# Kernel optimization log

Hardware: AMD Instinct MI355X
Metric: run time of the kernel (lower is better)

## Reference

```python
import jax, jax.numpy as jnp
import numpy as np

T, B, IN, H = 256, 256, 512, 512


def setup_inputs() -> dict:
    key = jax.random.key(0)
    k_x, k_d, k_ih, k_hh = jax.random.split(key, 4)
    x = jax.random.normal(k_x, (T, B, IN), dtype=jnp.float32)
    dones = jax.random.randint(k_d, (T, B), 0, 2, dtype=jnp.int32)
    # xavier_normal_ init as in the torch module (biases filled with 0)
    s_ih = (2.0 / (4 * H + IN)) ** 0.5
    s_hh = (2.0 / (4 * H + H)) ** 0.5
    W_ih = jax.random.normal(k_ih, (4 * H, IN), dtype=jnp.float32) * s_ih
    W_hh = jax.random.normal(k_hh, (4 * H, H), dtype=jnp.float32) * s_hh
    b_ih = jnp.zeros((4 * H,), dtype=jnp.float32)
    b_hh = jnp.zeros((4 * H,), dtype=jnp.float32)
    return {"x": x, "dones": dones, "W_ih": W_ih, "W_hh": W_hh,
            "b_ih": b_ih, "b_hh": b_hh}


def _lstm_scan(x, dones, W_ih, W_hh, b_ih, b_hh):
    # x: [T, B, IN], dones: [T, B]; single-layer LSTM, zero initial state.
    Bn = x.shape[1]
    Hn = W_hh.shape[1]
    h0 = jnp.zeros((Bn, Hn), dtype=x.dtype)
    c0 = jnp.zeros((Bn, Hn), dtype=x.dtype)
    b = b_ih + b_hh

    def step(carry, inp):
        h, c = carry
        x_t, d_t = inp
        keep = (1.0 - d_t.astype(x_t.dtype))[:, None]  # reset state where done
        h = h * keep
        c = c * keep
        pre = jnp.stack([h, c])  # [2, B, H] = concat(hidden, cell) before step
        gates = x_t @ W_ih.T + h @ W_hh.T + b  # [B, 4H], torch order i,f,g,o
        i, f, g, o = jnp.split(gates, 4, axis=-1)
        c_new = jax.nn.sigmoid(f) * c + jax.nn.sigmoid(i) * jnp.tanh(g)
        h_new = jax.nn.sigmoid(o) * jnp.tanh(c_new)
        return (h_new, c_new), (h_new, pre)

    _, (lstm_outputs, hidden_outputs) = jax.lax.scan(step, (h0, c0), (x, dones))
    # lstm_outputs: [T, B, H]; hidden_outputs: [T, 2*num_layers, B, H]
    return lstm_outputs, hidden_outputs


def reference(x, dones, W_ih, W_hh, b_ih, b_hh):
    return _lstm_scan(x, dones, W_ih, W_hh, b_ih, b_hh)
```

## Files before the change

### kernel.cpp

```cpp
#include <hip/hip_runtime.h>


#define T_STEPS 256
#define BATCH   256
#define INP     512
#define HID     512
#define GROUPS  8
#define MEMB    32
#define BT      32
#define NWG     (GROUPS*MEMB)
#define NTHR    256
#define XBUF    65536
#define K8OFF   (2*XBUF)
#define LDS_BYTES (2*XBUF + T_STEPS*BT)
#define PARM    0x40004000u

typedef float  f32x4  __attribute__((ext_vector_type(4)));
typedef short  bf16x8 __attribute__((ext_vector_type(8)));
typedef unsigned int u32x4 __attribute__((ext_vector_type(4)));

struct HF { u32x4 h[16]; };

typedef const __attribute__((address_space(1))) void gas_v;
typedef __attribute__((address_space(3))) void las_v;
__device__ __forceinline__ void gld_lds16(const void* g, void* l) {
  __builtin_amdgcn_global_load_lds((gas_v*)g, (las_v*)l, 16, 0, 0);
}

__device__ __forceinline__ unsigned short f2bf(float f) {
  unsigned u = __builtin_bit_cast(unsigned, f);
  return (unsigned short)((u + 0x8000u) >> 16);
}
__device__ __forceinline__ bf16x8 cvt8(float4 a, float4 b) {
  bf16x8 v;
  v[0]=(short)f2bf(a.x); v[1]=(short)f2bf(a.y); v[2]=(short)f2bf(a.z); v[3]=(short)f2bf(a.w);
  v[4]=(short)f2bf(b.x); v[5]=(short)f2bf(b.y); v[6]=(short)f2bf(b.z); v[7]=(short)f2bf(b.w);
  return v;
}
__device__ __forceinline__ float sigf(float x) {
  return __fdividef(1.0f, 1.0f + __expf(-x));
}
__device__ __forceinline__ float tanh_(float x) {
  float e = __expf(-2.0f * fabsf(x));
  float t = __fdividef(1.0f - e, 1.0f + e);
  return copysignf(t, x);
}
__device__ __forceinline__ f32x4 shflx4(f32x4 v, int m) {
  f32x4 r;
  r[0]=__shfl_xor(v[0],m,64); r[1]=__shfl_xor(v[1],m,64);
  r[2]=__shfl_xor(v[2],m,64); r[3]=__shfl_xor(v[3],m,64);
  return r;
}

__device__ __forceinline__ void llc_load_h(HF& o, const void* p) {
  unsigned long long a = (unsigned long long)p;
  asm volatile(
    "global_load_dwordx4 %[h0],  %[a], off sc0 sc1\n\t"
    "global_load_dwordx4 %[h1],  %[a], off offset:64 sc0 sc1\n\t"
    "global_load_dwordx4 %[h2],  %[a], off offset:128 sc0 sc1\n\t"
    "global_load_dwordx4 %[h3],  %[a], off offset:192 sc0 sc1\n\t"
    "global_load_dwordx4 %[h4],  %[a], off offset:256 sc0 sc1\n\t"
    "global_load_dwordx4 %[h5],  %[a], off offset:320 sc0 sc1\n\t"
    "global_load_dwordx4 %[h6],  %[a], off offset:384 sc0 sc1\n\t"
    "global_load_dwordx4 %[h7],  %[a], off offset:448 sc0 sc1\n\t"
    "global_load_dwordx4 %[h8],  %[a], off offset:512 sc0 sc1\n\t"
    "global_load_dwordx4 %[h9],  %[a], off offset:576 sc0 sc1\n\t"
    "global_load_dwordx4 %[h10], %[a], off offset:640 sc0 sc1\n\t"
    "global_load_dwordx4 %[h11], %[a], off offset:704 sc0 sc1\n\t"
    "global_load_dwordx4 %[h12], %[a], off offset:768 sc0 sc1\n\t"
    "global_load_dwordx4 %[h13], %[a], off offset:832 sc0 sc1\n\t"
    "global_load_dwordx4 %[h14], %[a], off offset:896 sc0 sc1\n\t"
    "global_load_dwordx4 %[h15], %[a], off offset:960 sc0 sc1\n\t"
    "s_waitcnt vmcnt(0)"
    : [h0]"=v"(o.h[0]),  [h1]"=v"(o.h[1]),  [h2]"=v"(o.h[2]),  [h3]"=v"(o.h[3]),
      [h4]"=v"(o.h[4]),  [h5]"=v"(o.h[5]),  [h6]"=v"(o.h[6]),  [h7]"=v"(o.h[7]),
      [h8]"=v"(o.h[8]),  [h9]"=v"(o.h[9]),  [h10]"=v"(o.h[10]),[h11]"=v"(o.h[11]),
      [h12]"=v"(o.h[12]),[h13]"=v"(o.h[13]),[h14]"=v"(o.h[14]),[h15]"=v"(o.h[15])
    : [a]"v"(a)
    : "memory");
}

__global__ void __launch_bounds__(NTHR, 1)
lstm_fused(const float* __restrict__ x, const int* __restrict__ dones,
           const float* __restrict__ Wih, const float* __restrict__ Whh,
           const float* __restrict__ bih, const float* __restrict__ bhh,
           float* __restrict__ out, unsigned* __restrict__ hb32,
           unsigned long long* __restrict__ hb64, int* __restrict__ flags)
{
  (void)flags;
  extern __shared__ char smem_raw[];
  unsigned short* wst   = (unsigned short*)smem_raw;
  char*           xring = smem_raw;
  unsigned char*  k8    = (unsigned char*)smem_raw + K8OFF;

  const int tid  = threadIdx.x;
  const int lane = tid & 63;
  const int wv   = tid >> 6;
  const int grp  = blockIdx.x >> 5;
  const int memb = blockIdx.x & 31;
  const int b0   = grp * BT;
  const int j0   = memb * 16;
  const int mtile = wv & 1;
  const int hh    = wv >> 1;
  const int q    = lane >> 4;
  const int n    = lane & 15;
  const int r    = n & 7;

  for (int e = tid; e < 64*1024; e += NTHR) {
    int s = e >> 10, k = e & 1023;
    int nf = s >> 4, nn = s & 15;
    int gp = nf & 1;
    int hloc = (nf >> 1)*8 + (nn & 7);
    int gate = (nn < 8) ? (gp ? 2 : 0) : (gp ? 3 : 1);
    int grow = gate*HID + j0 + hloc;
    float v = (k < INP) ? Wih[grow*INP + k] : Whh[grow*HID + (k - INP)];
    int kk = k >> 5, qq = (k >> 3) & 3, j = k & 7;
    wst[((kk*4 + nf)*64 + qq*16 + nn)*8 + j] = f2bf(v);
  }
  for (int idx = tid; idx < T_STEPS*BT; idx += NTHR) {
    int tt = idx >> 5, bb = idx & 31;
    k8[idx] = (unsigned char)(1 - dones[tt*BATCH + b0 + bb]);
  }
  __syncthreads();

  const int nf0 = 2*hh;
  bf16x8 B0[32], B1[32];
  #pragma unroll
  for (int kk = 0; kk < 32; ++kk) {
    B0[kk] = *(const bf16x8*)(wst + ((kk*4 + nf0    )*64 + lane)*8);
    B1[kk] = *(const bf16x8*)(wst + ((kk*4 + nf0 + 1)*64 + lane)*8);
  }
  __syncthreads();

  const int jmy = j0 + hh*8 + r;
  const float bi  = bih[0*HID + jmy] + bhh[0*HID + jmy];
  const float bf_ = bih[1*HID + jmy] + bhh[1*HID + jmy];
  const float bg  = bih[2*HID + jmy] + bhh[2*HID + jmy];
  const float bo  = bih[3*HID + jmy] + bhh[3*HID + jmy];

  float h_s[2] = {0.f, 0.f}, c_s[2] = {0.f, 0.f};
  const bool lo  = (n < 8);
  const int  rgb = lo ? 0 : 2;
  float* hidb = out + (size_t)T_STEPS*BATCH*HID;
  const int bbA = b0 + mtile*16 + n;

  auto stage_x = [&](int ts) {
    char* base = xring + (ts & 1)*XBUF + mtile*32768;
    const int lp   = lane ^ ((lane >> 3) & 1);
    const int row  = mtile*16 + ((lp >> 1) & 15);
    const int coff = ((lp >> 5) << 3) + (lp & 1)*4;
    const float* src0 = x + (size_t)(ts*BATCH + b0 + row)*INP + coff;
    #pragma unroll
    for (int e = 0; e < 32; ++e)
      gld_lds16(src0 + e*16, base + e*1024);
  };

  stage_x(0);
  asm volatile("s_waitcnt vmcnt(0)" ::: "memory");

  const char* xbase = xring + mtile*32768 + lane*32;
  const int   sx    = ((lane >> 2) & 1) << 4;

  for (int t = 0; t < T_STEPS; ++t) {
    f32x4 acc0 = {0.f,0.f,0.f,0.f}, acc1 = {0.f,0.f,0.f,0.f};
    const char* xb = xbase + (t & 1)*XBUF;
    #pragma unroll
    for (int kk = 0; kk < 16; ++kk) {
      float4 xa = *(const float4*)(xb + kk*2048 + sx);
      float4 xc = *(const float4*)(xb + kk*2048 + (16 ^ sx));
      bf16x8 a = cvt8(xa, xc);
      acc0 = __builtin_amdgcn_mfma_f32_16x16x32_bf16(a, B0[kk], acc0, 0, 0, 0);
      acc1 = __builtin_amdgcn_mfma_f32_16x16x32_bf16(a, B1[kk], acc1, 0, 0, 0);
    }

    const void* hbp = (const char*)(hb64 + ((t+1)&1)*(BATCH*HID/4)
                                  + (size_t)bbA*(HID/4)) + q*16;
    HF hf;
    llc_load_h(hf, hbp);

    if (t + 1 < T_STEPS) stage_x(t + 1);

    const int ebit = (t == 0) ? 1 : (((t - 1) >> 1) & 1);
    const unsigned want = ebit ? PARM : 0u;
    while (true) {
      unsigned bad = 0;
      #pragma unroll
      for (int kk = 0; kk < 16; ++kk) {
        u32x4 v = hf.h[kk];
        bad |= (v[0] ^ want) | (v[1] ^ want) | (v[2] ^ want) | (v[3] ^ want);
      }
      if (__all((bad & PARM) == 0u)) break;
      llc_load_h(hf, hbp);
    }

    const unsigned char kA = k8[t*BT + mtile*16 + n];
    const unsigned msk = kA ? (ebit ? ~PARM : 0xFFFFFFFFu) : 0u;
    #pragma unroll
    for (int kk = 0; kk < 16; ++kk) {
      u32x4 v = hf.h[kk];
      v[0] &= msk; v[1] &= msk; v[2] &= msk; v[3] &= msk;
      bf16x8 a = __builtin_bit_cast(bf16x8, v);
      acc0 = __builtin_amdgcn_mfma_f32_16x16x32_bf16(a, B0[16+kk], acc0, 0, 0, 0);
      acc1 = __builtin_amdgcn_mfma_f32_16x16x32_bf16(a, B1[16+kk], acc1, 0, 0, 0);
    }

    f32x4 oa = shflx4(acc0, 8), ob = shflx4(acc1, 8);
    f32x4 I = lo ? acc0 : oa;
    f32x4 F = lo ? oa : acc0;
    f32x4 G = lo ? acc1 : ob;
    f32x4 O = lo ? ob : acc1;

    float hnv[2], hrv[2], crv[2];
    #pragma unroll
    for (int u = 0; u < 2; ++u) {
      int rg = rgb + u;
      int lb = mtile*16 + q*4 + rg;
      float kp = (float)k8[t*BT + lb];
      float hr = h_s[u]*kp, cr = c_s[u]*kp;
      float iv  = sigf (I[rg] + bi);
      float fv_ = sigf (F[rg] + bf_);
      float gv  = tanh_(G[rg] + bg);
      float ov  = sigf (O[rg] + bo);
      float cn = fv_*cr + iv*gv;
      float hn = ov*tanh_(cn);
      h_s[u] = hn; c_s[u] = cn;
      hnv[u] = hn; hrv[u] = hr; crv[u] = cr;
    }

    {
      float send  = (n & 1) ? hnv[0] : hnv[1];
      float other = __shfl_xor(send, 1, 64);
      int lb0 = mtile*16 + q*4 + rgb;
      int lbm = (n & 1) ? lb0 + 1 : lb0;
      unsigned lo16 = (n & 1) ? (unsigned)f2bf(other)  : (unsigned)f2bf(hnv[0]);
      unsigned hi16 = (n & 1) ? (unsigned)f2bf(hnv[1]) : (unsigned)f2bf(other);
      unsigned dw = lo16 | (hi16 << 16);
      if ((t >> 1) & 1) dw |= PARM;
      unsigned* dst = hb32 + (t&1)*(BATCH*HID/2)
                    + (size_t)(b0 + lbm)*(HID/2) + (jmy >> 1);
      __hip_atomic_store(dst, dw, __ATOMIC_RELAXED, __HIP_MEMORY_SCOPE_AGENT);
    }

    #pragma unroll
    for (int u = 0; u < 2; ++u) {
      int lb = mtile*16 + q*4 + rgb + u;
      int bb = b0 + lb;
      out [(size_t)(t*BATCH + bb)*HID + jmy]       = hnv[u];
      hidb[((size_t)(t*2+0)*BATCH + bb)*HID + jmy] = hrv[u];
      hidb[((size_t)(t*2+1)*BATCH + bb)*HID + jmy] = crv[u];
    }
  }
}

extern "C" void kernel_launch(void* const* d_in, const int* in_sizes, int n_in,
                              void* d_out, int out_size, void* d_ws, size_t ws_size,
                              hipStream_t stream) {
  (void)in_sizes; (void)n_in; (void)out_size; (void)ws_size;
  const float* x   = (const float*)d_in[0];
  const int*   dn  = (const int*)  d_in[1];
  const float* Wih = (const float*)d_in[2];
  const float* Whh = (const float*)d_in[3];
  const float* bih = (const float*)d_in[4];
  const float* bhh = (const float*)d_in[5];
  float* out = (float*)d_out;

  unsigned*           hb32 = (unsigned*)d_ws;
  unsigned long long* hb64 = (unsigned long long*)d_ws;
  size_t hbuf_bytes = (size_t)2*BATCH*HID*sizeof(unsigned short);
  int* flags = (int*)((char*)d_ws + hbuf_bytes);

  hipMemsetAsync(d_ws, 0x40, hbuf_bytes, stream);
  hipFuncSetAttribute((const void*)lstm_fused,
                      hipFuncAttributeMaxDynamicSharedMemorySize, LDS_BYTES);
  lstm_fused<<<dim3(NWG), dim3(NTHR), LDS_BYTES, stream>>>(
      x, dn, Wih, Whh, bih, bhh, out, hb32, hb64, flags);
}
```

Measured before the change: 2.020 ms.

## Overlap hidden-state loads with input MFMAs and add flag-based polling fallback

The recurrent h loads and the next x staging are now issued at the top of each step, so their latency overlaps the input-projection MFMAs. The old loop that repeatedly reloaded the full 1 KB parity-tagged h until it was fresh is replaced by a one-shot freshness check. If that check fails, the wave polls small per-wave progress flags with s_sleep and then reloads h once. Each wave now publishes a step counter after draining its h stores, which adds a vmcnt wait and an extra atomic store per step. The change also uses the v_cvt_pk_bf16_f32 instruction, which rounds to nearest-even rather than the old manual half-up rounding, and splits the MFMA accumulators into even/odd chains to shorten dependency chains.

Result: slower. 3.093 ms (+53.1%).

```diff
diff --git a/kernel.cpp b/kernel.cpp
--- a/kernel.cpp
+++ b/kernel.cpp
@@ -18,6 +18,7 @@
 typedef float  f32x4  __attribute__((ext_vector_type(4)));
 typedef short  bf16x8 __attribute__((ext_vector_type(8)));
 typedef unsigned int u32x4 __attribute__((ext_vector_type(4)));
+typedef unsigned int u32x2 __attribute__((ext_vector_type(2)));
 
 struct HF { u32x4 h[16]; };
 
@@ -31,11 +32,13 @@
   unsigned u = __builtin_bit_cast(unsigned, f);
   return (unsigned short)((u + 0x8000u) >> 16);
 }
-__device__ __forceinline__ bf16x8 cvt8(float4 a, float4 b) {
-  bf16x8 v;
-  v[0]=(short)f2bf(a.x); v[1]=(short)f2bf(a.y); v[2]=(short)f2bf(a.z); v[3]=(short)f2bf(a.w);
-  v[4]=(short)f2bf(b.x); v[5]=(short)f2bf(b.y); v[6]=(short)f2bf(b.z); v[7]=(short)f2bf(b.w);
-  return v;
+__device__ __forceinline__ bf16x8 cvt8pk(float4 a, float4 b) {
+  union { unsigned u[4]; bf16x8 v; } r;
+  asm("v_cvt_pk_bf16_f32 %0, %1, %2" : "=v"(r.u[0]) : "v"(a.x), "v"(a.y));
+  asm("v_cvt_pk_bf16_f32 %0, %1, %2" : "=v"(r.u[1]) : "v"(a.z), "v"(a.w));
+  asm("v_cvt_pk_bf16_f32 %0, %1, %2" : "=v"(r.u[2]) : "v"(b.x), "v"(b.y));
+  asm("v_cvt_pk_bf16_f32 %0, %1, %2" : "=v"(r.u[3]) : "v"(b.z), "v"(b.w));
+  return r.v;
 }
 __device__ __forceinline__ float sigf(float x) {
   return __fdividef(1.0f, 1.0f + __expf(-x));
@@ -52,7 +55,7 @@
   return r;
 }
 
-__device__ __forceinline__ void llc_load_h(HF& o, const void* p) {
+__device__ __forceinline__ void llc_issue_h(HF& o, const void* p) {
   unsigned long long a = (unsigned long long)p;
   asm volatile(
     "global_load_dwordx4 %[h0],  %[a], off sc0 sc1\n\t"
@@ -70,14 +73,23 @@
     "global_load_dwordx4 %[h12], %[a], off offset:768 sc0 sc1\n\t"
     "global_load_dwordx4 %[h13], %[a], off offset:832 sc0 sc1\n\t"
     "global_load_dwordx4 %[h14], %[a], off offset:896 sc0 sc1\n\t"
-    "global_load_dwordx4 %[h15], %[a], off offset:960 sc0 sc1\n\t"
-    "s_waitcnt vmcnt(0)"
+    "global_load_dwordx4 %[h15], %[a], off offset:960 sc0 sc1"
     : [h0]"=v"(o.h[0]),  [h1]"=v"(o.h[1]),  [h2]"=v"(o.h[2]),  [h3]"=v"(o.h[3]),
       [h4]"=v"(o.h[4]),  [h5]"=v"(o.h[5]),  [h6]"=v"(o.h[6]),  [h7]"=v"(o.h[7]),
       [h8]"=v"(o.h[8]),  [h9]"=v"(o.h[9]),  [h10]"=v"(o.h[10]),[h11]"=v"(o.h[11]),
       [h12]"=v"(o.h[12]),[h13]"=v"(o.h[13]),[h14]"=v"(o.h[14]),[h15]"=v"(o.h[15])
     : [a]"v"(a)
     : "memory");
+}
+__device__ __forceinline__ u32x2 flag_issue(const void* p) {
+  u32x2 f; unsigned long long a = (unsigned long long)p;
+  asm volatile("global_load_dwordx2 %0, %1, off sc0 sc1"
+               : "=v"(f) : "v"(a) : "memory");
+  return f;
+}
+__device__ __forceinline__ void vmwait0() {
+  asm volatile("s_waitcnt vmcnt(0)" ::: "memory");
+  __builtin_amdgcn_sched_barrier(0);
 }
 
 __global__ void __launch_bounds__(NTHR, 1)
@@ -87,7 +99,6 @@
            float* __restrict__ out, unsigned* __restrict__ hb32,
            unsigned long long* __restrict__ hb64, int* __restrict__ flags)
 {
-  (void)flags;
   extern __shared__ char smem_raw[];
   unsigned short* wst   = (unsigned short*)smem_raw;
   char*           xring = smem_raw;
@@ -144,6 +155,9 @@
   float* hidb = out + (size_t)T_STEPS*BATCH*HID;
   const int bbA = b0 + mtile*16 + n;
 
+  int* myflag = flags + blockIdx.x*4 + wv;
+  const int* fp2 = flags + grp*128 + 2*lane;
+
   auto stage_x = [&](int ts) {
     char* base = xring + (ts & 1)*XBUF + mtile*32768;
     const int lp   = lane ^ ((lane >> 3) & 1);
@@ -156,53 +170,83 @@
   };
 
   stage_x(0);
-  asm volatile("s_waitcnt vmcnt(0)" ::: "memory");
+  vmwait0();
 
   const char* xbase = xring + mtile*32768 + lane*32;
   const int   sx    = ((lane >> 2) & 1) << 4;
+  const f32x4 zf4 = {0.f,0.f,0.f,0.f};
 
   for (int t = 0; t < T_STEPS; ++t) {
-    f32x4 acc0 = {0.f,0.f,0.f,0.f}, acc1 = {0.f,0.f,0.f,0.f};
+    const void* hbp = (const char*)(hb64 + ((t+1)&1)*(BATCH*HID/4)
+                                  + (size_t)bbA*(HID/4)) + q*16;
+    u32x2 flv = flag_issue(fp2);
+    HF hf;
+    llc_issue_h(hf, hbp);
+    if (t + 1 < T_STEPS) stage_x(t + 1);
+
+    f32x4 a0e = zf4, a0o = zf4, a1e = zf4, a1o = zf4;
     const char* xb = xbase + (t & 1)*XBUF;
     #pragma unroll
-    for (int kk = 0; kk < 16; ++kk) {
+    for (int kk = 0; kk < 16; kk += 2) {
       float4 xa = *(const float4*)(xb + kk*2048 + sx);
       float4 xc = *(const float4*)(xb + kk*2048 + (16 ^ sx));
-      bf16x8 a = cvt8(xa, xc);
-      acc0 = __builtin_amdgcn_mfma_f32_16x16x32_bf16(a, B0[kk], acc0, 0, 0, 0);
-      acc1 = __builtin_amdgcn_mfma_f32_16x16x32_bf16(a, B1[kk], acc1, 0, 0, 0);
-    }
-
-    const void* hbp = (const char*)(hb64 + ((t+1)&1)*(BATCH*HID/4)
-                                  + (size_t)bbA*(HID/4)) + q*16;
-    HF hf;
-    llc_load_h(hf, hbp);
-
-    if (t + 1 < T_STEPS) stage_x(t + 1);
-
+      bf16x8 ae = cvt8pk(xa, xc);
+      a0e = __builtin_amdgcn_mfma_f32_16x16x32_bf16(ae, B0[kk], a0e, 0, 0, 0);
+      a1e = __builtin_amdgcn_mfma_f32_16x16x32_bf16(ae, B1[kk], a1e, 0, 0, 0);
+      float4 xd = *(const float4*)(xb + (kk+1)*2048 + sx);
+      float4 xe = *(const float4*)(xb + (kk+1)*2048 + (16 ^ sx));
+      bf16x8 ao = cvt8pk(xd, xe);
+      a0o = __builtin_amdgcn_mfma_f32_16x16x32_bf16(ao, B0[kk+1], a0o, 0, 0, 0);
+      a1o = __builtin_amdgcn_mfma_f32_16x16x32_bf16(ao, B1[kk+1], a1o, 0, 0, 0);
+    }
+
+    vmwait0();
     const int ebit = (t == 0) ? 1 : (((t - 1) >> 1) & 1);
-    const unsigned want = ebit ? PARM : 0u;
-    while (true) {
-      unsigned bad = 0;
+    bool fresh;
+    if (ebit) {
+      unsigned acc = 0xFFFFFFFFu;
       #pragma unroll
       for (int kk = 0; kk < 16; ++kk) {
         u32x4 v = hf.h[kk];
-        bad |= (v[0] ^ want) | (v[1] ^ want) | (v[2] ^ want) | (v[3] ^ want);
+        acc &= v[0] & v[1] & v[2] & v[3];
       }
-      if (__all((bad & PARM) == 0u)) break;
-      llc_load_h(hf, hbp);
+      fresh = __all((acc & PARM) == PARM);
+    } else {
+      unsigned acc = 0u;
+      #pragma unroll
+      for (int kk = 0; kk < 16; ++kk) {
+        u32x4 v = hf.h[kk];
+        acc |= v[0] | v[1] | v[2] | v[3];
+      }
+      fresh = __all((acc & PARM) == 0u);
+    }
+    if (!fresh) {
+      u32x2 f = flv;
+      while (!__all(((int)f[0] >= t) && ((int)f[1] >= t))) {
+        __builtin_amdgcn_s_sleep(1);
+        f = flag_issue(fp2);
+        vmwait0();
+      }
+      llc_issue_h(hf, hbp);
+      vmwait0();
     }
 
     const unsigned char kA = k8[t*BT + mtile*16 + n];
     const unsigned msk = kA ? (ebit ? ~PARM : 0xFFFFFFFFu) : 0u;
     #pragma unroll
-    for (int kk = 0; kk < 16; ++kk) {
+    for (int kk = 0; kk < 16; kk += 2) {
       u32x4 v = hf.h[kk];
       v[0] &= msk; v[1] &= msk; v[2] &= msk; v[3] &= msk;
-      bf16x8 a = __builtin_bit_cast(bf16x8, v);
-      acc0 = __builtin_amdgcn_mfma_f32_16x16x32_bf16(a, B0[16+kk], acc0, 0, 0, 0);
-      acc1 = __builtin_amdgcn_mfma_f32_16x16x32_bf16(a, B1[16+kk], acc1, 0, 0, 0);
-    }
+      bf16x8 ae = __builtin_bit_cast(bf16x8, v);
+      a0e = __builtin_amdgcn_mfma_f32_16x16x32_bf16(ae, B0[16+kk], a0e, 0, 0, 0);
+      a1e = __builtin_amdgcn_mfma_f32_16x16x32_bf16(ae, B1[16+kk], a1e, 0, 0, 0);
+      u32x4 w = hf.h[kk+1];
+      w[0] &= msk; w[1] &= msk; w[2] &= msk; w[3] &= msk;
+      bf16x8 ao = __builtin_bit_cast(bf16x8, w);
+      a0o = __builtin_amdgcn_mfma_f32_16x16x32_bf16(ao, B0[17+kk], a0o, 0, 0, 0);
+      a1o = __builtin_amdgcn_mfma_f32_16x16x32_bf16(ao, B1[17+kk], a1o, 0, 0, 0);
+    }
+    f32x4 acc0 = a0e + a0o, acc1 = a1e + a1o;
 
     f32x4 oa = shflx4(acc0, 8), ob = shflx4(acc1, 8);
     f32x4 I = lo ? acc0 : oa;
@@ -232,15 +276,19 @@
       float other = __shfl_xor(send, 1, 64);
       int lb0 = mtile*16 + q*4 + rgb;
       int lbm = (n & 1) ? lb0 + 1 : lb0;
-      unsigned lo16 = (n & 1) ? (unsigned)f2bf(other)  : (unsigned)f2bf(hnv[0]);
-      unsigned hi16 = (n & 1) ? (unsigned)f2bf(hnv[1]) : (unsigned)f2bf(other);
-      unsigned dw = lo16 | (hi16 << 16);
+      float vlo = (n & 1) ? other  : hnv[0];
+      float vhi = (n & 1) ? hnv[1] : other;
+      unsigned dw;
+      asm("v_cvt_pk_bf16_f32 %0, %1, %2" : "=v"(dw) : "v"(vlo), "v"(vhi));
       if ((t >> 1) & 1) dw |= PARM;
       unsigned* dst = hb32 + (t&1)*(BATCH*HID/2)
                     + (size_t)(b0 + lbm)*(HID/2) + (jmy >> 1);
       __hip_atomic_store(dst, dw, __ATOMIC_RELAXED, __HIP_MEMORY_SCOPE_AGENT);
     }
 
+    vmwait0();
+    __hip_atomic_store(myflag, t + 1,
+                       __ATOMIC_RELAXED, __HIP_MEMORY_SCOPE_AGENT);
     #pragma unroll
     for (int u = 0; u < 2; ++u) {
       int lb = mtile*16 + q*4 + rgb + u;
@@ -270,6 +318,7 @@
   int* flags = (int*)((char*)d_ws + hbuf_bytes);
 
   hipMemsetAsync(d_ws, 0x40, hbuf_bytes, stream);
+  hipMemsetAsync(flags, 0, NWG*4*sizeof(int), stream);
   hipFuncSetAttribute((const void*)lstm_fused,
                       hipFuncAttributeMaxDynamicSharedMemorySize, LDS_BYTES);
   lstm_fused<<<dim3(NWG), dim3(NTHR), LDS_BYTES, stream>>>(
```
